# Optimization experiments

Hardware: AMD Instinct MI355X
Metric: run time of the kernel (lower is better)

## Reference

```python
import jax, jax.numpy as jnp
import numpy as np

N = 50000
D = 128
E = 600000


def setup_inputs() -> dict:
    key = jax.random.key(0)
    k1, k2, k3, k4, k5, k6 = jax.random.split(key, 6)
    x = jax.random.normal(k1, (N, D), dtype=jnp.float32)
    edge_index = jax.random.randint(k2, (2, E), 0, N, dtype=jnp.int32)
    s = 1.0 / np.sqrt(D)
    W1 = jax.random.uniform(k3, (D, D), dtype=jnp.float32, minval=-s, maxval=s)
    b1 = jax.random.uniform(k4, (D,), dtype=jnp.float32, minval=-s, maxval=s)
    W2 = jax.random.uniform(k5, (D, D), dtype=jnp.float32, minval=-s, maxval=s)
    b2 = jax.random.uniform(k6, (D,), dtype=jnp.float32, minval=-s, maxval=s)
    return {"x": x, "edge_index": edge_index, "W1": W1, "b1": b1, "W2": W2, "b2": b2}


def _gcn_conv(x, src, dst, W, b):
    # PyG GCNConv (default flow source->target): out[dst] += norm * (x @ W)[src] + b
    n = x.shape[0]
    deg = jax.ops.segment_sum(jnp.ones_like(dst, dtype=x.dtype), dst, num_segments=n)
    dinv = jnp.where(deg > 0, jax.lax.rsqrt(deg), 0.0)
    norm = dinv[src] * dinv[dst]          # [E+N]
    h = x @ W                             # [N, D]
    msg = h[src] * norm[:, None]          # [E+N, D] gather + scale
    out = jax.ops.segment_sum(msg, dst, num_segments=n)
    return out + b


def reference(x, edge_index, W1, b1, W2, b2):
    n = x.shape[0]
    loops = jnp.arange(n, dtype=edge_index.dtype)
    src = jnp.concatenate([edge_index[0], loops])  # add self-loops
    dst = jnp.concatenate([edge_index[1], loops])
    h = jax.nn.relu(_gcn_conv(x, src, dst, W1, b1))
    out = jax.nn.relu(_gcn_conv(h, src, dst, W2, b2))
    return out
```

## Files before the change

kernel.cpp:

```cpp
#include <hip/hip_runtime.h>
#include <stdint.h>

typedef __attribute__((ext_vector_type(8))) short bf16x8;
typedef __attribute__((ext_vector_type(4))) float f32x4;

#define CAP 64

__device__ __forceinline__ float bf2f(unsigned int u) {
    union { unsigned int i; float f; } v; v.i = u << 16; return v.f;
}
__device__ __forceinline__ unsigned short f2bf(float f) {
    union { float f; unsigned int i; } v; v.f = f;
    unsigned int b = v.i;
    b += 0x7FFFu + ((b >> 16) & 1u);
    return (unsigned short)(b >> 16);
}


__global__ void bucket_kernel(const int* __restrict__ src, const int* __restrict__ dst,
                              int* __restrict__ counts, unsigned short* __restrict__ bucket,
                              int E) {
    int e = blockIdx.x * blockDim.x + threadIdx.x;
    if (e < E) {
        int s = src[e], d = dst[e];
        int slot = atomicAdd(&counts[d], 1);
        if (slot < CAP) bucket[(size_t)d * CAP + slot] = (unsigned short)s;
    }
}


__global__ void conv_w_dinv(const float* __restrict__ W1, const float* __restrict__ W2,
                            unsigned short* __restrict__ Wt1, unsigned short* __restrict__ Wt2,
                            const int* __restrict__ counts, float* __restrict__ dinv, int N) {
    int t = blockIdx.x * 256 + threadIdx.x;
    if (t < 32768) {
        const float* W = (t < 16384) ? W1 : W2;
        unsigned short* O = (t < 16384) ? Wt1 : Wt2;
        int i = t & 16383;
        int n = i >> 7, k = i & 127;
        O[i] = f2bf(W[k * 128 + n]);
    } else {
        int n = t - 32768;
        if (n < N) dinv[n] = rsqrtf((float)(counts[n] + 1));
    }
}


template <bool A_BF16>
__global__ __launch_bounds__(256) void gemm128(const void* __restrict__ Av,
                                               const unsigned short* __restrict__ Wt,
                                               const float* __restrict__ dinv,
                                               unsigned short* __restrict__ G, int M) {
    int t = threadIdx.x;
    int wave = t >> 6, lane = t & 63;
    int m0 = (blockIdx.x * 4 + wave) * 16;
    int mrow = lane & 15, quad = lane >> 4;

    int arow = m0 + mrow;
    int srow = arow < M ? arow : M - 1;

    f32x4 acc[8];
#pragma unroll
    for (int nt = 0; nt < 8; ++nt) acc[nt] = (f32x4){0.f, 0.f, 0.f, 0.f};

#pragma unroll
    for (int kb = 0; kb < 4; ++kb) {
        bf16x8 a;
        if (A_BF16) {
            const unsigned short* Arow = (const unsigned short*)Av + (size_t)srow * 128;
            a = *(const bf16x8*)(Arow + kb * 32 + quad * 8);
        } else {
            const float* Arow = (const float*)Av + (size_t)srow * 128;
            f32x4 lo = *(const f32x4*)(Arow + kb * 32 + quad * 8);
            f32x4 hi = *(const f32x4*)(Arow + kb * 32 + quad * 8 + 4);
#pragma unroll
            for (int i = 0; i < 4; ++i) { a[i] = (short)f2bf(lo[i]); a[i + 4] = (short)f2bf(hi[i]); }
        }
#pragma unroll
        for (int nt = 0; nt < 8; ++nt) {
            bf16x8 b = *(const bf16x8*)(Wt + (size_t)(nt * 16 + mrow) * 128 + kb * 32 + quad * 8);
            acc[nt] = __builtin_amdgcn_mfma_f32_16x16x32_bf16(a, b, acc[nt], 0, 0, 0);
        }
    }

#pragma unroll
    for (int r = 0; r < 4; ++r) {
        int row = m0 + quad * 4 + r;
        if (row < M) {
            float dr = dinv[row];
#pragma unroll
            for (int nt = 0; nt < 8; ++nt)
                G[(size_t)row * 128 + nt * 16 + mrow] = f2bf(acc[nt][r] * dr);
        }
    }
}


template <bool OUT_BF16>
__global__ __launch_bounds__(256) void agg_kernel(const unsigned short* __restrict__ g,
                                                  const int* __restrict__ counts,
                                                  const unsigned short* __restrict__ bucket,
                                                  const float* __restrict__ dinv,
                                                  const float* __restrict__ bias,
                                                  void* __restrict__ out, int N) {
    int wave = threadIdx.x >> 6, lane = threadIdx.x & 63;
    int half = lane >> 5, hl = lane & 31;
    int n = blockIdx.x * 8 + wave * 2 + half;
    bool valid = n < N;
    int nc = valid ? n : N - 1;

    const uint2* g2 = (const uint2*)g;
    const unsigned short* brow = bucket + (size_t)nc * CAP;
    int sa = brow[hl];
    int sb = brow[hl + 32];
    int deg = counts[nc];
    float di = dinv[nc];
    int m = min(deg, CAP);
    int lb = half << 5;

    uint2 hv = g2[(size_t)nc * 32 + hl];
    float a0 = bf2f(hv.x & 0xFFFFu);
    float a1 = bf2f(hv.x >> 16);
    float a2 = bf2f(hv.y & 0xFFFFu);
    float a3 = bf2f(hv.y >> 16);
    float c0 = 0.f, c1 = 0.f, c2 = 0.f, c3 = 0.f;

    auto process = [&](int sl, int cnt) {
#pragma unroll 1
        for (int j = 0; j < cnt; j += 16) {
            int s[16]; float w[16]; uint2 v[16];
#pragma unroll
            for (int u = 0; u < 16; ++u) {
                int idx = j + u;
                bool ok = idx < cnt;
                s[u] = __shfl(sl, lb + (ok ? idx : 0));
                w[u] = ok ? 1.f : 0.f;
            }
#pragma unroll
            for (int u = 0; u < 16; ++u) v[u] = g2[(size_t)s[u] * 32 + hl];
#pragma unroll
            for (int u = 0; u < 16; ++u) {
                if (u & 1) {
                    c0 = fmaf(w[u], bf2f(v[u].x & 0xFFFFu), c0);
                    c1 = fmaf(w[u], bf2f(v[u].x >> 16), c1);
                    c2 = fmaf(w[u], bf2f(v[u].y & 0xFFFFu), c2);
                    c3 = fmaf(w[u], bf2f(v[u].y >> 16), c3);
                } else {
                    a0 = fmaf(w[u], bf2f(v[u].x & 0xFFFFu), a0);
                    a1 = fmaf(w[u], bf2f(v[u].x >> 16), a1);
                    a2 = fmaf(w[u], bf2f(v[u].y & 0xFFFFu), a2);
                    a3 = fmaf(w[u], bf2f(v[u].y >> 16), a3);
                }
            }
        }
    };

    process(sa, min(m, 32));
    if (m > 32) process(sb, m - 32);

    f32x4 bv = ((const f32x4*)bias)[hl];
    float o0 = fmaxf((a0 + c0) * di + bv[0], 0.f);
    float o1 = fmaxf((a1 + c1) * di + bv[1], 0.f);
    float o2 = fmaxf((a2 + c2) * di + bv[2], 0.f);
    float o3 = fmaxf((a3 + c3) * di + bv[3], 0.f);

    if (valid) {
        if (OUT_BF16) {
            uint2 o;
            o.x = (unsigned int)f2bf(o0) | ((unsigned int)f2bf(o1) << 16);
            o.y = (unsigned int)f2bf(o2) | ((unsigned int)f2bf(o3) << 16);
            ((uint2*)out)[(size_t)n * 32 + hl] = o;
        } else {
            ((f32x4*)out)[(size_t)n * 32 + hl] = (f32x4){o0, o1, o2, o3};
        }
    }
}


extern "C" void kernel_launch(void* const* d_in, const int* in_sizes, int n_in,
                              void* d_out, int out_size, void* d_ws, size_t ws_size,
                              hipStream_t stream) {
    const float* x  = (const float*)d_in[0];
    const int*   ei = (const int*)d_in[1];
    const float* W1 = (const float*)d_in[2];
    const float* b1 = (const float*)d_in[3];
    const float* W2 = (const float*)d_in[4];
    const float* b2 = (const float*)d_in[5];
    float* out = (float*)d_out;

    int N = in_sizes[0] / 128;
    int E = in_sizes[1] / 2;
    const int* src = ei;
    const int* dst = ei + E;

    char* p = (char*)d_ws;
    auto alloc = [&](size_t bytes) {
        char* r = p; p += (bytes + 255) & ~(size_t)255; return r;
    };
    int*            counts = (int*)           alloc((size_t)N * 4);
    float*          dinv   = (float*)         alloc((size_t)N * 4);
    unsigned short* bucket = (unsigned short*)alloc((size_t)N * CAP * 2);
    unsigned short* g1     = (unsigned short*)alloc((size_t)N * 128 * 2);
    unsigned short* out1   = (unsigned short*)alloc((size_t)N * 128 * 2);
    unsigned short* Wt1    = (unsigned short*)alloc(16384 * 2);
    unsigned short* Wt2    = (unsigned short*)alloc(16384 * 2);

    hipMemsetAsync(counts, 0, (size_t)N * 4, stream);
    bucket_kernel<<<(E + 255) / 256, 256, 0, stream>>>(src, dst, counts, bucket, E);
    conv_w_dinv<<<(32768 + N + 255) / 256, 256, 0, stream>>>(W1, W2, Wt1, Wt2, counts, dinv, N);

    int gblocks = (N + 63) / 64;
    gemm128<false><<<gblocks, 256, 0, stream>>>(x, Wt1, dinv, g1, N);
    agg_kernel<true><<<(N + 7) / 8, 256, 0, stream>>>(g1, counts, bucket, dinv, b1, out1, N);
    gemm128<true><<<gblocks, 256, 0, stream>>>(out1, Wt2, dinv, g1, N);
    agg_kernel<false><<<(N + 7) / 8, 256, 0, stream>>>(g1, counts, bucket, dinv, b2, out, N);
}
```

Before: 216.6 us.

## Fuse weight conversion into bucketing, compute dinv inline, one node per wave

Folds the weight transpose/convert into the edge-bucketing kernel and drops the separate dinv kernel and buffer, computing rsqrt(deg+1) on the fly in the GEMM epilogue and aggregation. The aggregation kernel now gives each node a full wave: each lane handles two features with 4-byte gathers, and neighbor indices are broadcast with readlane instead of shuffles. This removes one launch and the dinv memory traffic and makes the neighbor index scalar, at the cost of narrower per-lane loads and half as many nodes per block.

After: 213.3 us. About the same (-1.5%).

```diff
diff --git a/kernel.cpp b/kernel.cpp
--- a/kernel.cpp
+++ b/kernel.cpp
@@ -9,39 +9,30 @@
 __device__ __forceinline__ float bf2f(unsigned int u) {
     union { unsigned int i; float f; } v; v.i = u << 16; return v.f;
 }
-__device__ __forceinline__ unsigned short f2bf(float f) {
+__device__ __forceinline__ unsigned int f2bf(float f) {
     union { float f; unsigned int i; } v; v.f = f;
     unsigned int b = v.i;
     b += 0x7FFFu + ((b >> 16) & 1u);
-    return (unsigned short)(b >> 16);
+    return b >> 16;
 }
 
 
 __global__ void bucket_kernel(const int* __restrict__ src, const int* __restrict__ dst,
                               int* __restrict__ counts, unsigned short* __restrict__ bucket,
-                              int E) {
-    int e = blockIdx.x * blockDim.x + threadIdx.x;
-    if (e < E) {
-        int s = src[e], d = dst[e];
-        int slot = atomicAdd(&counts[d], 1);
-        if (slot < CAP) bucket[(size_t)d * CAP + slot] = (unsigned short)s;
-    }
-}
-
-
-__global__ void conv_w_dinv(const float* __restrict__ W1, const float* __restrict__ W2,
-                            unsigned short* __restrict__ Wt1, unsigned short* __restrict__ Wt2,
-                            const int* __restrict__ counts, float* __restrict__ dinv, int N) {
+                              int E,
+                              const float* __restrict__ W1, const float* __restrict__ W2,
+                              unsigned short* __restrict__ Wt1, unsigned short* __restrict__ Wt2) {
     int t = blockIdx.x * 256 + threadIdx.x;
     if (t < 32768) {
         const float* W = (t < 16384) ? W1 : W2;
         unsigned short* O = (t < 16384) ? Wt1 : Wt2;
         int i = t & 16383;
-        int n = i >> 7, k = i & 127;
-        O[i] = f2bf(W[k * 128 + n]);
-    } else {
-        int n = t - 32768;
-        if (n < N) dinv[n] = rsqrtf((float)(counts[n] + 1));
+        O[i] = (unsigned short)f2bf(W[(i & 127) * 128 + (i >> 7)]);
+    }
+    if (t < E) {
+        int s = src[t], d = dst[t];
+        int slot = atomicAdd(&counts[d], 1);
+        if (slot < CAP) bucket[(size_t)d * CAP + slot] = (unsigned short)s;
     }
 }
 
@@ -49,7 +40,7 @@
 template <bool A_BF16>
 __global__ __launch_bounds__(256) void gemm128(const void* __restrict__ Av,
                                                const unsigned short* __restrict__ Wt,
-                                               const float* __restrict__ dinv,
+                                               const int* __restrict__ counts,
                                                unsigned short* __restrict__ G, int M) {
     int t = threadIdx.x;
     int wave = t >> 6, lane = t & 63;
@@ -87,10 +78,10 @@
     for (int r = 0; r < 4; ++r) {
         int row = m0 + quad * 4 + r;
         if (row < M) {
-            float dr = dinv[row];
+            float dr = rsqrtf((float)counts[row] + 1.0f);
 #pragma unroll
             for (int nt = 0; nt < 8; ++nt)
-                G[(size_t)row * 128 + nt * 16 + mrow] = f2bf(acc[nt][r] * dr);
+                G[(size_t)row * 128 + nt * 16 + mrow] = (unsigned short)f2bf(acc[nt][r] * dr);
         }
     }
 }
@@ -100,79 +91,57 @@
 __global__ __launch_bounds__(256) void agg_kernel(const unsigned short* __restrict__ g,
                                                   const int* __restrict__ counts,
                                                   const unsigned short* __restrict__ bucket,
-                                                  const float* __restrict__ dinv,
                                                   const float* __restrict__ bias,
                                                   void* __restrict__ out, int N) {
-    int wave = threadIdx.x >> 6, lane = threadIdx.x & 63;
-    int half = lane >> 5, hl = lane & 31;
-    int n = blockIdx.x * 8 + wave * 2 + half;
-    bool valid = n < N;
-    int nc = valid ? n : N - 1;
+    int lane = threadIdx.x & 63;
+    int n = blockIdx.x * 4 + (threadIdx.x >> 6);
+    if (n >= N) return;
 
-    const uint2* g2 = (const uint2*)g;
-    const unsigned short* brow = bucket + (size_t)nc * CAP;
-    int sa = brow[hl];
-    int sb = brow[hl + 32];
-    int deg = counts[nc];
-    float di = dinv[nc];
+    const unsigned int* g32 = (const unsigned int*)g;
+    int deg = counts[n];
     int m = min(deg, CAP);
-    int lb = half << 5;
+    float di = rsqrtf((float)deg + 1.0f);
+    int sv = bucket[(size_t)n * CAP + lane];
 
-    uint2 hv = g2[(size_t)nc * 32 + hl];
-    float a0 = bf2f(hv.x & 0xFFFFu);
-    float a1 = bf2f(hv.x >> 16);
-    float a2 = bf2f(hv.y & 0xFFFFu);
-    float a3 = bf2f(hv.y >> 16);
-    float c0 = 0.f, c1 = 0.f, c2 = 0.f, c3 = 0.f;
+    unsigned int hv = g32[(size_t)n * 64 + lane];
+    float a0 = bf2f(hv & 0xFFFFu);
+    float a1 = bf2f(hv >> 16);
+    float c0 = 0.f, c1 = 0.f;
 
-    auto process = [&](int sl, int cnt) {
 #pragma unroll 1
-        for (int j = 0; j < cnt; j += 16) {
-            int s[16]; float w[16]; uint2 v[16];
+    for (int j0 = 0; j0 < m; j0 += 16) {
+        const unsigned int* rp[16];
+        float w[16];
 #pragma unroll
-            for (int u = 0; u < 16; ++u) {
-                int idx = j + u;
-                bool ok = idx < cnt;
-                s[u] = __shfl(sl, lb + (ok ? idx : 0));
-                w[u] = ok ? 1.f : 0.f;
-            }
+        for (int u = 0; u < 16; ++u) {
+            int idx = j0 + u;
+            int cid = idx < m ? idx : m - 1;
+            int s = __builtin_amdgcn_readlane(sv, cid);
+            rp[u] = g32 + (size_t)s * 64;
+            w[u] = idx < m ? 1.f : 0.f;
+        }
+        unsigned int v[16];
 #pragma unroll
-            for (int u = 0; u < 16; ++u) v[u] = g2[(size_t)s[u] * 32 + hl];
+        for (int u = 0; u < 16; ++u) v[u] = rp[u][lane];
 #pragma unroll
-            for (int u = 0; u < 16; ++u) {
-                if (u & 1) {
-                    c0 = fmaf(w[u], bf2f(v[u].x & 0xFFFFu), c0);
-                    c1 = fmaf(w[u], bf2f(v[u].x >> 16), c1);
-                    c2 = fmaf(w[u], bf2f(v[u].y & 0xFFFFu), c2);
-                    c3 = fmaf(w[u], bf2f(v[u].y >> 16), c3);
-                } else {
-                    a0 = fmaf(w[u], bf2f(v[u].x & 0xFFFFu), a0);
-                    a1 = fmaf(w[u], bf2f(v[u].x >> 16), a1);
-                    a2 = fmaf(w[u], bf2f(v[u].y & 0xFFFFu), a2);
-                    a3 = fmaf(w[u], bf2f(v[u].y >> 16), a3);
-                }
+        for (int u = 0; u < 16; ++u) {
+            if (u & 1) {
+                c0 = fmaf(w[u], bf2f(v[u] & 0xFFFFu), c0);
+                c1 = fmaf(w[u], bf2f(v[u] >> 16), c1);
+            } else {
+                a0 = fmaf(w[u], bf2f(v[u] & 0xFFFFu), a0);
+                a1 = fmaf(w[u], bf2f(v[u] >> 16), a1);
             }
         }
-    };
+    }
 
-    process(sa, min(m, 32));
-    if (m > 32) process(sb, m - 32);
-
-    f32x4 bv = ((const f32x4*)bias)[hl];
-    float o0 = fmaxf((a0 + c0) * di + bv[0], 0.f);
-    float o1 = fmaxf((a1 + c1) * di + bv[1], 0.f);
-    float o2 = fmaxf((a2 + c2) * di + bv[2], 0.f);
-    float o3 = fmaxf((a3 + c3) * di + bv[3], 0.f);
-
-    if (valid) {
-        if (OUT_BF16) {
-            uint2 o;
-            o.x = (unsigned int)f2bf(o0) | ((unsigned int)f2bf(o1) << 16);
-            o.y = (unsigned int)f2bf(o2) | ((unsigned int)f2bf(o3) << 16);
-            ((uint2*)out)[(size_t)n * 32 + hl] = o;
-        } else {
-            ((f32x4*)out)[(size_t)n * 32 + hl] = (f32x4){o0, o1, o2, o3};
-        }
+    float2 bv = ((const float2*)bias)[lane];
+    float o0 = fmaxf((a0 + c0) * di + bv.x, 0.f);
+    float o1 = fmaxf((a1 + c1) * di + bv.y, 0.f);
+    if (OUT_BF16) {
+        ((unsigned int*)out)[(size_t)n * 64 + lane] = f2bf(o0) | (f2bf(o1) << 16);
+    } else {
+        ((float2*)out)[(size_t)n * 64 + lane] = make_float2(o0, o1);
     }
 }
 
@@ -198,7 +167,6 @@
         char* r = p; p += (bytes + 255) & ~(size_t)255; return r;
     };
     int*            counts = (int*)           alloc((size_t)N * 4);
-    float*          dinv   = (float*)         alloc((size_t)N * 4);
     unsigned short* bucket = (unsigned short*)alloc((size_t)N * CAP * 2);
     unsigned short* g1     = (unsigned short*)alloc((size_t)N * 128 * 2);
     unsigned short* out1   = (unsigned short*)alloc((size_t)N * 128 * 2);
@@ -206,12 +174,12 @@
     unsigned short* Wt2    = (unsigned short*)alloc(16384 * 2);
 
     hipMemsetAsync(counts, 0, (size_t)N * 4, stream);
-    bucket_kernel<<<(E + 255) / 256, 256, 0, stream>>>(src, dst, counts, bucket, E);
-    conv_w_dinv<<<(32768 + N + 255) / 256, 256, 0, stream>>>(W1, W2, Wt1, Wt2, counts, dinv, N);
+    bucket_kernel<<<(E + 255) / 256, 256, 0, stream>>>(src, dst, counts, bucket, E,
+                                                       W1, W2, Wt1, Wt2);
 
     int gblocks = (N + 63) / 64;
-    gemm128<false><<<gblocks, 256, 0, stream>>>(x, Wt1, dinv, g1, N);
-    agg_kernel<true><<<(N + 7) / 8, 256, 0, stream>>>(g1, counts, bucket, dinv, b1, out1, N);
-    gemm128<true><<<gblocks, 256, 0, stream>>>(out1, Wt2, dinv, g1, N);
-    agg_kernel<false><<<(N + 7) / 8, 256, 0, stream>>>(g1, counts, bucket, dinv, b2, out, N);
+    gemm128<false><<<gblocks, 256, 0, stream>>>(x, Wt1, counts, g1, N);
+    agg_kernel<true><<<(N + 3) / 4, 256, 0, stream>>>(g1, counts, bucket, b1, out1, N);
+    gemm128<true><<<gblocks, 256, 0, stream>>>(out1, Wt2, counts, g1, N);
+    agg_kernel<false><<<(N + 3) / 4, 256, 0, stream>>>(g1, counts, bucket, b2, out, N);
 }
```
